# Kernel optimization log

Measured on AMD Instinct MI355X. Metric: run time of the kernel, lower is better.

Reference implementation:

```python
import jax, jax.numpy as jnp
import numpy as np

T, Z, D_DIM = 8, 2048, 1024
N_EXP, P_SLOT, H = 64, 32, 1024
LN_EPS = 1e-5


def setup_inputs() -> dict:
    key = jax.random.key(0)
    k = jax.random.split(key, 5)
    s = 0.02
    return {
        "x": jax.random.normal(k[0], (T, Z, D_DIM), dtype=jnp.float32),
        "phi_w": jax.random.normal(k[1], (N_EXP * P_SLOT, D_DIM), dtype=jnp.float32) * s,
        "phi_b": jax.random.normal(k[2], (N_EXP * P_SLOT,), dtype=jnp.float32) * s,
        "expert_w": jax.random.normal(k[3], (N_EXP, D_DIM, H), dtype=jnp.float32) * s,
        "expert_b": jax.random.normal(k[4], (N_EXP, H), dtype=jnp.float32) * s,
    }


def reference(x, phi_w, phi_b, expert_w, expert_b):
    t, z, d = x.shape
    n = expert_w.shape[0]
    p = phi_w.shape[0] // n
    # routing logits: [t, z, n, p]
    logits = (jnp.einsum('tzd,ed->tze', x, phi_w) + phi_b).reshape(t, z, n, p)
    D = jax.nn.softmax(logits, axis=3)  # dispatch: softmax over slots p
    C = jax.nn.softmax(logits, axis=2)  # combine:  softmax over experts n
    # slot inputs, summed over batch AND tokens (as in the source einsum)
    X_tilde = jnp.einsum('tznp,tzd->npd', D, x)
    X_tilde = jnp.clip(X_tilde, -33000.0, 65000.0)
    # layer norm over last dim, no affine
    mu = jnp.mean(X_tilde, axis=-1, keepdims=True)
    var = jnp.mean(jnp.square(X_tilde - mu), axis=-1, keepdims=True)
    X_tilde = (X_tilde - mu) * jax.lax.rsqrt(var + LN_EPS)
    X_tilde = jnp.tanh(X_tilde)
    # per-expert Linear, batched over experts: [n,p,d] x [n,d,H] -> [n,p,H]
    Y_tilde = jnp.einsum('npd,ndH->npH', X_tilde, expert_w) + expert_b[:, None, :]
    # combine back to tokens: [t,z,H]
    Y = jnp.einsum('tznp,npH->tzH', C, Y_tilde)
    return Y
```

## Files before the change

kernel.cpp:

```cpp
#include <hip/hip_runtime.h>
#include <hip/hip_bf16.h>
#include <math.h>

#define TOKENS   16384
#define DDIM     1024
#define NEXP     64
#define PSLOT    32
#define NSLOTS   2048
#define HDIM     1024
#define LN_EPS   1e-5f
#define KSPLIT   8

typedef __bf16 b16x8 __attribute__((ext_vector_type(8)));
typedef float  f32x4 __attribute__((ext_vector_type(4)));

__device__ __forceinline__ unsigned short f2b(float f) {
    union { float f; unsigned u; } v; v.f = f;
    unsigned r = v.u + 0x7FFF + ((v.u >> 16) & 1);
    return (unsigned short)(r >> 16);
}

__device__ __forceinline__ void load_lds16(const void* g, void* l) {
    __builtin_amdgcn_global_load_lds(
        (const __attribute__((address_space(1))) void*)g,
        (__attribute__((address_space(3))) void*)l, 16, 0, 0);
}

template<bool BIAS>
__global__ __launch_bounds__(512, 2) void gemm_nt_256(
    const unsigned short* __restrict__ A,
    const unsigned short* __restrict__ B,
    const float* __restrict__ bias,
    float* __restrict__ C,
    int M, int N, int K)
{
    __shared__ unsigned short lds[2][2][256 * 64];
    const int tid  = threadIdx.x;
    const int wave = tid >> 6;
    const int lane = tid & 63;
    const int wr = wave >> 2;
    const int wc = wave & 3;
    const int fr = lane & 15;
    const int fs = lane >> 4;
    const int kswz = ((lane & 7) ^ (lane >> 3)) * 8;

    const int gx  = (int)gridDim.x, gy = (int)gridDim.y;
    const int nwg = gx * gy;
    const int wg  = (int)blockIdx.y * gx + (int)blockIdx.x;
    const int swz = (wg & 7) * (nwg >> 3) + (wg >> 3);
    const int m0 = (swz / gx) * 256;
    const int n0 = (swz % gx) * 256;

    const int kc = K / gridDim.z;
    const int kb = blockIdx.z * kc;
    C += (size_t)blockIdx.z * M * N;
    const int NT = kc >> 6;

    f32x4 acc[8][4] = {};
    b16x8 Ag[4][2], Bf[2][2], Bs2[2][2];

#define KOF(T)   (kb + (T) * 64)

#define STAGE_A(BUF, T, R0) { \
    const int k0_ = KOF(T); \
    _Pragma("unroll") for (int hh = 0; hh < 2; ++hh) { \
        const int rp_ = (R0) + hh * 64 + wave * 8 + (lane >> 3); \
        const int L_  = ((rp_ >> 6) & 1) * 128 + ((rp_ >> 7) & 1) * 64 + (rp_ & 63); \
        load_lds16(A + (size_t)(m0 + L_) * K + k0_ + kswz, \
                   &lds[BUF][0][((R0) + hh * 64 + wave * 8) * 64]); } }

#define STAGE_B(BUF, T, R0) { \
    const int k0_ = KOF(T); \
    _Pragma("unroll") for (int hh = 0; hh < 2; ++hh) { \
        const int rp_ = (R0) + hh * 64 + wave * 8 + (lane >> 3); \
        const int L_  = ((rp_ >> 5) & 3) * 64 + ((rp_ >> 7) & 1) * 32 + (rp_ & 31); \
        load_lds16(B + (size_t)(n0 + L_) * K + k0_ + kswz, \
                   &lds[BUF][1][((R0) + hh * 64 + wave * 8) * 64]); } }

#define LDA_G(BUF, IBASE) \
    _Pragma("unroll") for (int ii = 0; ii < 4; ++ii) { \
        const int rp_ = (IBASE) + 64 * wr + ii * 16 + fr; \
        _Pragma("unroll") for (int h = 0; h < 2; ++h) \
            Ag[ii][h] = *(const b16x8*)&lds[BUF][0][rp_ * 64 + (((h * 4 + fs) ^ (rp_ & 7)) * 8)]; }

#define LDB_G(BUF, JBASE, DST) \
    _Pragma("unroll") for (int jj = 0; jj < 2; ++jj) { \
        const int rp_ = (JBASE) + 32 * wc + jj * 16 + fr; \
        _Pragma("unroll") for (int h = 0; h < 2; ++h) \
            DST[jj][h] = *(const b16x8*)&lds[BUF][1][rp_ * 64 + (((h * 4 + fs) ^ (rp_ & 7)) * 8)]; }

#define MFMA_Q(IB, JB, BREG) \
    __builtin_amdgcn_s_setprio(1); \
    _Pragma("unroll") for (int ii = 0; ii < 4; ++ii) \
    _Pragma("unroll") for (int jj = 0; jj < 2; ++jj) \
    _Pragma("unroll") for (int h = 0; h < 2; ++h) \
        acc[(IB) + ii][(JB) + jj] = __builtin_amdgcn_mfma_f32_16x16x32_bf16( \
            Ag[ii][h], BREG[jj][h], acc[(IB) + ii][(JB) + jj], 0, 0, 0); \
    __builtin_amdgcn_s_setprio(0);

#define BAR1  { __builtin_amdgcn_s_barrier(); __builtin_amdgcn_sched_barrier(0); }
#define BAR2  { __builtin_amdgcn_s_barrier(); }
#define VMW6  { asm volatile("s_waitcnt vmcnt(6)" ::: "memory"); \
                __builtin_amdgcn_sched_barrier(0); }
#define VMW0  { asm volatile("s_waitcnt vmcnt(0)" ::: "memory"); \
                __builtin_amdgcn_sched_barrier(0); }

    STAGE_A(0, 0, 0);   STAGE_B(0, 0, 0);   STAGE_B(0, 0, 128);  STAGE_A(0, 0, 128);
    STAGE_A(1, 1, 0);   STAGE_B(1, 1, 0);   STAGE_B(1, 1, 128);
    VMW6; BAR2;

    const int nit = NT >> 1;
    for (int it = 0; it < nit - 1; ++it) {
        const int t1 = 2 * it + 1;
        LDA_G(0, 0); LDB_G(0, 0, Bf);
        STAGE_A(1, t1, 128);
        BAR1; MFMA_Q(0, 0, Bf); BAR2;
        LDB_G(0, 128, Bs2);
        STAGE_A(0, t1 + 1, 0);
        BAR1; MFMA_Q(0, 2, Bs2); BAR2;
        LDA_G(0, 128);
        STAGE_B(0, t1 + 1, 0);
        BAR1; MFMA_Q(4, 2, Bs2); BAR2;
        STAGE_B(0, t1 + 1, 128);
        BAR1; MFMA_Q(4, 0, Bf); VMW6; BAR2;
        LDA_G(1, 0); LDB_G(1, 0, Bf);
        STAGE_A(0, t1 + 1, 128);
        BAR1; MFMA_Q(0, 0, Bf); BAR2;
        LDB_G(1, 128, Bs2);
        STAGE_A(1, t1 + 2, 0);
        BAR1; MFMA_Q(0, 2, Bs2); BAR2;
        LDA_G(1, 128);
        STAGE_B(1, t1 + 2, 0);
        BAR1; MFMA_Q(4, 2, Bs2); BAR2;
        STAGE_B(1, t1 + 2, 128);
        BAR1; MFMA_Q(4, 0, Bf); VMW6; BAR2;
    }

    {
        const int t1 = NT - 1;
        LDA_G(0, 0); LDB_G(0, 0, Bf);
        STAGE_A(1, t1, 128);
        BAR1; MFMA_Q(0, 0, Bf); BAR2;
        LDB_G(0, 128, Bs2);
        BAR1; MFMA_Q(0, 2, Bs2); BAR2;
        LDA_G(0, 128);
        BAR1; MFMA_Q(4, 2, Bs2); BAR2;
        BAR1; MFMA_Q(4, 0, Bf); VMW0; BAR2;
        LDA_G(1, 0); LDB_G(1, 0, Bf);
        BAR1; MFMA_Q(0, 0, Bf); BAR2;
        LDB_G(1, 128, Bs2);
        BAR1; MFMA_Q(0, 2, Bs2); BAR2;
        LDA_G(1, 128);
        BAR1; MFMA_Q(4, 2, Bs2); BAR2;
        BAR1; MFMA_Q(4, 0, Bf); BAR2;
    }

    const int col  = lane & 15;
    const int row4 = (lane >> 4) * 4;
#pragma unroll
    for (int j = 0; j < 4; ++j) {
        const int n = n0 + wc * 64 + j * 16 + col;
        const float bj = BIAS ? bias[n] : 0.f;
#pragma unroll
        for (int i = 0; i < 8; ++i) {
#pragma unroll
            for (int r = 0; r < 4; ++r) {
                const int m = m0 + wr * 128 + i * 16 + row4 + r;
                C[(size_t)m * N + n] = acc[i][j][r] + bj;
            }
        }
    }
#undef KOF
#undef STAGE_A
#undef STAGE_B
#undef LDA_G
#undef LDB_G
#undef MFMA_Q
#undef BAR1
#undef BAR2
#undef VMW6
#undef VMW0
}

__global__ __launch_bounds__(256) void prep_x(
    const float* __restrict__ in, unsigned short* __restrict__ xb,
    unsigned short* __restrict__ xT)
{
    __shared__ unsigned short tile[64][68];
    const int t  = threadIdx.x;
    const int c0 = blockIdx.x * 64;
    const int r0 = blockIdx.y * 64;
    const int tr = t >> 4, tc4 = (t & 15) * 4;
#pragma unroll
    for (int i = 0; i < 4; ++i) {
        const int r = tr + i * 16;
        const float4 v = *(const float4*)&in[(size_t)(r0 + r) * DDIM + c0 + tc4];
        ushort4 o;
        o.x = f2b(v.x); o.y = f2b(v.y); o.z = f2b(v.z); o.w = f2b(v.w);
        *(ushort4*)&xb[(size_t)(r0 + r) * DDIM + c0 + tc4] = o;
        tile[tc4 + 0][r] = o.x; tile[tc4 + 1][r] = o.y;
        tile[tc4 + 2][r] = o.z; tile[tc4 + 3][r] = o.w;
    }
    __syncthreads();
#pragma unroll
    for (int i = 0; i < 4; ++i) {
        const int r = tr + i * 16;
        ushort4 o;
        o.x = tile[r][tc4 + 0]; o.y = tile[r][tc4 + 1];
        o.z = tile[r][tc4 + 2]; o.w = tile[r][tc4 + 3];
        *(ushort4*)&xT[(size_t)(c0 + r) * TOKENS + r0 + tc4] = o;
    }
}

__global__ __launch_bounds__(256) void cast_f32_bf16(
    const float* __restrict__ in, unsigned short* __restrict__ out)
{
    const size_t i = (size_t)(blockIdx.x * 256 + threadIdx.x) * 8;
    const float4 a = *(const float4*)&in[i];
    const float4 b = *(const float4*)&in[i + 4];
    ushort4 o0, o1;
    o0.x = f2b(a.x); o0.y = f2b(a.y); o0.z = f2b(a.z); o0.w = f2b(a.w);
    o1.x = f2b(b.x); o1.y = f2b(b.y); o1.z = f2b(b.z); o1.w = f2b(b.w);
    *(ushort4*)&out[i]     = o0;
    *(ushort4*)&out[i + 4] = o1;
}

__global__ __launch_bounds__(256) void dispatch_T(
    const float* __restrict__ logits, unsigned short* __restrict__ DbT)
{
    __shared__ float ls[8 * 1057];
    const int tid  = threadIdx.x;
    const int tok0 = blockIdx.x * 32;
    const int s0   = blockIdx.y * 256;

#pragma unroll
    for (int i = 0; i < 8; ++i) {
        const int flat = i * 256 + tid;
        const int row  = flat >> 6;
        const int c4   = (flat & 63) * 4;
        const float4 v = *(const float4*)&logits[(size_t)(tok0 + row) * NSLOTS + s0 + c4];
        float* b = &ls[(c4 >> 5) * 1057 + row * 33 + (c4 & 31)];
        b[0] = v.x; b[1] = v.y; b[2] = v.z; b[3] = v.w;
    }
    __syncthreads();

    const int tok = tid & 31, n = tid >> 5;
    const float* r = &ls[n * 1057 + tok * 33];
    float m = r[0];
#pragma unroll
    for (int p = 1; p < PSLOT; ++p) m = fmaxf(m, r[p]);
    float s = 0.f;
#pragma unroll
    for (int p = 0; p < PSLOT; ++p) s += __expf(r[p] - m);
    const float inv = 1.f / s;
    unsigned short* o = &DbT[(size_t)(s0 + n * 32) * TOKENS + tok0 + tok];
#pragma unroll
    for (int p = 0; p < PSLOT; ++p)
        o[(size_t)p * TOKENS] = f2b(__expf(r[p] - m) * inv);
}

__global__ __launch_bounds__(256) void combine_softmax(
    const float* __restrict__ logits, unsigned short* __restrict__ Cb)
{
    __shared__ float ls[NEXP * 33];
    __shared__ float pm[8][32], ps[8][32];
    const int tid = threadIdx.x;
    const size_t base = (size_t)blockIdx.x * NSLOTS;

#pragma unroll
    for (int i = 0; i < 8; ++i) {
        const int e = tid + i * 256;
        ls[e + (e >> 5)] = logits[base + e];
    }
    __syncthreads();

    const int p = tid & 31, sub = tid >> 5;
    float m = ls[(sub * 8) * 33 + p];
#pragma unroll
    for (int k = 1; k < 8; ++k) m = fmaxf(m, ls[(sub * 8 + k) * 33 + p]);
    float s = 0.f;
#pragma unroll
    for (int k = 0; k < 8; ++k) s += __expf(ls[(sub * 8 + k) * 33 + p] - m);
    pm[sub][p] = m; ps[sub][p] = s;
    __syncthreads();

    float M = pm[0][p];
#pragma unroll
    for (int k = 1; k < 8; ++k) M = fmaxf(M, pm[k][p]);
    float S = 0.f;
#pragma unroll
    for (int k = 0; k < 8; ++k) S += ps[k][p] * __expf(pm[k][p] - M);
    const float cinv = 1.f / S;

#pragma unroll
    for (int k = 0; k < 8; ++k) {
        const int n = sub * 8 + k;
        Cb[base + n * 32 + p] = f2b(__expf(ls[n * 33 + p] - M) * cinv);
    }
}

__global__ __launch_bounds__(256) void reduce_ln_tanh(
    const float* __restrict__ parts, float* __restrict__ Xt)
{
    const int tid = threadIdx.x;
    const size_t off = (size_t)blockIdx.x * DDIM + tid * 4;
    __shared__ float red1[4], red2[4];

    float4 v = *(const float4*)&parts[off];
#pragma unroll
    for (int s = 1; s < KSPLIT; ++s) {
        const float4 p = *(const float4*)&parts[(size_t)s * NSLOTS * DDIM + off];
        v.x += p.x; v.y += p.y; v.z += p.z; v.w += p.w;
    }
    v.x = fminf(fmaxf(v.x, -33000.f), 65000.f);
    v.y = fminf(fmaxf(v.y, -33000.f), 65000.f);
    v.z = fminf(fmaxf(v.z, -33000.f), 65000.f);
    v.w = fminf(fmaxf(v.w, -33000.f), 65000.f);

    float s = v.x + v.y + v.z + v.w;
#pragma unroll
    for (int off2 = 32; off2 > 0; off2 >>= 1) s += __shfl_down(s, off2);
    if ((tid & 63) == 0) red1[tid >> 6] = s;
    __syncthreads();
    const float mu = (red1[0] + red1[1] + red1[2] + red1[3]) * (1.f / DDIM);

    const float dx = v.x - mu, dy = v.y - mu, dz = v.z - mu, dw = v.w - mu;
    float q = dx * dx + dy * dy + dz * dz + dw * dw;
#pragma unroll
    for (int off2 = 32; off2 > 0; off2 >>= 1) q += __shfl_down(q, off2);
    if ((tid & 63) == 0) red2[tid >> 6] = q;
    __syncthreads();
    const float var = (red2[0] + red2[1] + red2[2] + red2[3]) * (1.f / DDIM);
    const float sc = rsqrtf(var + LN_EPS);

    float4 o;
    o.x = tanhf(dx * sc); o.y = tanhf(dy * sc);
    o.z = tanhf(dz * sc); o.w = tanhf(dw * sc);
    *(float4*)&Xt[off] = o;
}

__global__ __launch_bounds__(256) void expert_gemm(
    const float* __restrict__ Xt, const float* __restrict__ W,
    const float* __restrict__ bias, unsigned short* __restrict__ YtT)
{
    const int n   = blockIdx.y;
    const int h0  = blockIdx.x * 64;
    const int tid = threadIdx.x;
    __shared__ float As[32][17];
    __shared__ float Bs[16][68];
    __shared__ unsigned short ty[64][36];

    const int r  = tid >> 3;
    const int c8 = (tid & 7) * 8;
    float acc[8];
#pragma unroll
    for (int j = 0; j < 8; ++j) acc[j] = 0.f;

    const float* Wn = W + (size_t)n * DDIM * HDIM;
    for (int k0 = 0; k0 < DDIM; k0 += 16) {
        if (tid < 128) {
            const int row = tid >> 2, c4 = (tid & 3) * 4;
            const float4 v = *(const float4*)&Xt[(size_t)(n * 32 + row) * DDIM + k0 + c4];
            As[row][c4 + 0] = v.x; As[row][c4 + 1] = v.y;
            As[row][c4 + 2] = v.z; As[row][c4 + 3] = v.w;
        }
        {
            const int row = tid >> 4, c4 = (tid & 15) * 4;
            *(float4*)&Bs[row][c4] =
                *(const float4*)&Wn[(size_t)(k0 + row) * HDIM + h0 + c4];
        }
        __syncthreads();
#pragma unroll
        for (int kk = 0; kk < 16; ++kk) {
            const float a = As[r][kk];
            const float4 b0 = *(const float4*)&Bs[kk][c8];
            const float4 b1 = *(const float4*)&Bs[kk][c8 + 4];
            acc[0] = fmaf(a, b0.x, acc[0]); acc[1] = fmaf(a, b0.y, acc[1]);
            acc[2] = fmaf(a, b0.z, acc[2]); acc[3] = fmaf(a, b0.w, acc[3]);
            acc[4] = fmaf(a, b1.x, acc[4]); acc[5] = fmaf(a, b1.y, acc[5]);
            acc[6] = fmaf(a, b1.z, acc[6]); acc[7] = fmaf(a, b1.w, acc[7]);
        }
        __syncthreads();
    }

    const float* bn = bias + (size_t)n * HDIM + h0;
#pragma unroll
    for (int j = 0; j < 8; ++j)
        ty[c8 + j][r] = f2b(acc[j] + bn[c8 + j]);
    __syncthreads();

    const int row = tid >> 2, q = (tid & 3) * 8;
    const ushort4 u0 = *(const ushort4*)&ty[row][q];
    const ushort4 u1 = *(const ushort4*)&ty[row][q + 4];
    unsigned short* dst = &YtT[(size_t)(h0 + row) * NSLOTS + n * 32 + q];
    *(ushort4*)&dst[0] = u0;
    *(ushort4*)&dst[4] = u1;
}

extern "C" void kernel_launch(void* const* d_in, const int* in_sizes, int n_in,
                              void* d_out, int out_size, void* d_ws, size_t ws_size,
                              hipStream_t stream)
{
    const float* x        = (const float*)d_in[0];
    const float* phi_w    = (const float*)d_in[1];
    const float* phi_b    = (const float*)d_in[2];
    const float* expert_w = (const float*)d_in[3];
    const float* expert_b = (const float*)d_in[4];
    float* out = (float*)d_out;

    char* ws = (char*)d_ws;
    const size_t MB = 1u << 20;
    unsigned short* xb     = (unsigned short*)(ws);
    unsigned short* xT     = (unsigned short*)(ws +  32 * MB);
    unsigned short* pwb    = (unsigned short*)(ws +  64 * MB);
    float*          logits = (float*)(ws +  68 * MB);
    unsigned short* DbT    = (unsigned short*)(ws + 196 * MB);
    unsigned short* Cb     = (unsigned short*)(ws + 260 * MB);
    float*          parts  = (float*)(ws + 324 * MB);
    float*          Xt     = (float*)(ws + 388 * MB);
    unsigned short* YtT    = (unsigned short*)(ws + 396 * MB);

    prep_x<<<dim3(DDIM / 64, TOKENS / 64), 256, 0, stream>>>(x, xb, xT);
    cast_f32_bf16<<<NSLOTS * DDIM / (256 * 8), 256, 0, stream>>>(phi_w, pwb);

    gemm_nt_256<true><<<dim3(NSLOTS / 256, TOKENS / 256), 512, 0, stream>>>(
        xb, pwb, phi_b, logits, TOKENS, NSLOTS, DDIM);

    dispatch_T<<<dim3(TOKENS / 32, NSLOTS / 256), 256, 0, stream>>>(logits, DbT);

    combine_softmax<<<TOKENS, 256, 0, stream>>>(logits, Cb);

    gemm_nt_256<false>
        <<<dim3(DDIM / 256, NSLOTS / 256, KSPLIT), 512, 0, stream>>>(
            DbT, xT, nullptr, parts, NSLOTS, DDIM, TOKENS);

    reduce_ln_tanh<<<NSLOTS, 256, 0, stream>>>(parts, Xt);

    expert_gemm<<<dim3(HDIM / 64, NEXP), 256, 0, stream>>>(
        Xt, expert_w, expert_b, YtT);

    gemm_nt_256<false><<<dim3(HDIM / 256, TOKENS / 256), 512, 0, stream>>>(
        Cb, YtT, nullptr, out, TOKENS, HDIM, NSLOTS);
}
```

Baseline: 780.6 us.

## Fuse dispatch and combine softmaxes into one kernel with online expert softmax

```diff
diff --git a/kernel.cpp b/kernel.cpp
--- a/kernel.cpp
+++ b/kernel.cpp
@@ -225,77 +225,93 @@
     *(ushort4*)&out[i + 4] = o1;
 }
 
-__global__ __launch_bounds__(256) void dispatch_T(
-    const float* __restrict__ logits, unsigned short* __restrict__ DbT)
-{
-    __shared__ float ls[8 * 1057];
+__global__ __launch_bounds__(256) void softmax_both(
+    const float* __restrict__ logits,
+    unsigned short* __restrict__ DbT, unsigned short* __restrict__ Cb)
+{
+    __shared__ float ls[8][32][33];
+    __shared__ float Mv[32][33], Sv[32][33];
     const int tid  = threadIdx.x;
     const int tok0 = blockIdx.x * 32;
-    const int s0   = blockIdx.y * 256;
-
-#pragma unroll
-    for (int i = 0; i < 8; ++i) {
-        const int flat = i * 256 + tid;
-        const int row  = flat >> 6;
-        const int c4   = (flat & 63) * 4;
-        const float4 v = *(const float4*)&logits[(size_t)(tok0 + row) * NSLOTS + s0 + c4];
-        float* b = &ls[(c4 >> 5) * 1057 + row * 33 + (c4 & 31)];
-        b[0] = v.x; b[1] = v.y; b[2] = v.z; b[3] = v.w;
-    }
-    __syncthreads();
-
-    const int tok = tid & 31, n = tid >> 5;
-    const float* r = &ls[n * 1057 + tok * 33];
-    float m = r[0];
-#pragma unroll
-    for (int p = 1; p < PSLOT; ++p) m = fmaxf(m, r[p]);
-    float s = 0.f;
-#pragma unroll
-    for (int p = 0; p < PSLOT; ++p) s += __expf(r[p] - m);
-    const float inv = 1.f / s;
-    unsigned short* o = &DbT[(size_t)(s0 + n * 32) * TOKENS + tok0 + tok];
-#pragma unroll
-    for (int p = 0; p < PSLOT; ++p)
-        o[(size_t)p * TOKENS] = f2b(__expf(r[p] - m) * inv);
-}
-
-__global__ __launch_bounds__(256) void combine_softmax(
-    const float* __restrict__ logits, unsigned short* __restrict__ Cb)
-{
-    __shared__ float ls[NEXP * 33];
-    __shared__ float pm[8][32], ps[8][32];
-    const int tid = threadIdx.x;
-    const size_t base = (size_t)blockIdx.x * NSLOTS;
-
-#pragma unroll
-    for (int i = 0; i < 8; ++i) {
-        const int e = tid + i * 256;
-        ls[e + (e >> 5)] = logits[base + e];
-    }
-    __syncthreads();
-
-    const int p = tid & 31, sub = tid >> 5;
-    float m = ls[(sub * 8) * 33 + p];
-#pragma unroll
-    for (int k = 1; k < 8; ++k) m = fmaxf(m, ls[(sub * 8 + k) * 33 + p]);
-    float s = 0.f;
-#pragma unroll
-    for (int k = 0; k < 8; ++k) s += __expf(ls[(sub * 8 + k) * 33 + p] - m);
-    pm[sub][p] = m; ps[sub][p] = s;
-    __syncthreads();
-
-    float M = pm[0][p];
-#pragma unroll
-    for (int k = 1; k < 8; ++k) M = fmaxf(M, pm[k][p]);
-    float S = 0.f;
-#pragma unroll
-    for (int k = 0; k < 8; ++k) S += ps[k][p] * __expf(pm[k][p] - M);
-    const float cinv = 1.f / S;
-
-#pragma unroll
-    for (int k = 0; k < 8; ++k) {
-        const int n = sub * 8 + k;
-        Cb[base + n * 32 + p] = f2b(__expf(ls[n * 33 + p] - M) * cinv);
+    const int tok  = tid & 31;
+
+    {
+        const int tk = tid >> 3, pp = (tid & 7) * 4;
+#pragma unroll
+        for (int q = 0; q < 4; ++q) { Mv[tk][pp + q] = -1e30f; Sv[tk][pp + q] = 0.f; }
+    }
+    __syncthreads();
+
+    for (int c = 0; c < 8; ++c) {
+#pragma unroll
+        for (int i = 0; i < 8; ++i) {
+            const int flat = i * 256 + tid;
+            const int row  = flat >> 6;
+            const int c4   = (flat & 63) * 4;
+            const float4 v = *(const float4*)&logits[(size_t)(tok0 + row) * NSLOTS + c * 256 + c4];
+            float* b = &ls[c4 >> 5][row][c4 & 31];
+            b[0] = v.x; b[1] = v.y; b[2] = v.z; b[3] = v.w;
+        }
+        __syncthreads();
+
+        {
+            const int nl = tid >> 5;
+            const float* r = ls[nl][tok];
+            float m = r[0];
+#pragma unroll
+            for (int p = 1; p < PSLOT; ++p) m = fmaxf(m, r[p]);
+            float s = 0.f;
+#pragma unroll
+            for (int p = 0; p < PSLOT; ++p) s += __expf(r[p] - m);
+            const float inv = 1.f / s;
+            unsigned short* o = &DbT[(size_t)(c * 256 + nl * 32) * TOKENS + tok0 + tok];
+#pragma unroll
+            for (int p = 0; p < PSLOT; ++p)
+                o[(size_t)p * TOKENS] = f2b(__expf(r[p] - m) * inv);
+        }
+
+        {
+            const int pg = tid >> 5;
+#pragma unroll
+            for (int k = 0; k < 4; ++k) {
+                const int p = pg * 4 + k;
+                float m8 = ls[0][tok][p];
+#pragma unroll
+                for (int n = 1; n < 8; ++n) m8 = fmaxf(m8, ls[n][tok][p]);
+                float s8 = 0.f;
+#pragma unroll
+                for (int n = 0; n < 8; ++n) s8 += __expf(ls[n][tok][p] - m8);
+                const float M = Mv[tok][p], S = Sv[tok][p];
+                const float Mn = fmaxf(M, m8);
+                Sv[tok][p] = S * __expf(M - Mn) + s8 * __expf(m8 - Mn);
+                Mv[tok][p] = Mn;
+            }
+        }
+        __syncthreads();
+    }
+
+    {
+        const int tk = tid >> 3, pp = (tid & 7) * 4;
+#pragma unroll
+        for (int q = 0; q < 4; ++q) Sv[tk][pp + q] = 1.f / Sv[tk][pp + q];
+    }
+    __syncthreads();
+
+    for (int c = 0; c < 8; ++c) {
+#pragma unroll
+        for (int i = 0; i < 8; ++i) {
+            const int flat = i * 256 + tid;
+            const int row  = flat >> 6;
+            const int c4   = (flat & 63) * 4;
+            const int p    = c4 & 31;
+            const float4 v = *(const float4*)&logits[(size_t)(tok0 + row) * NSLOTS + c * 256 + c4];
+            ushort4 o;
+            o.x = f2b(__expf(v.x - Mv[row][p + 0]) * Sv[row][p + 0]);
+            o.y = f2b(__expf(v.y - Mv[row][p + 1]) * Sv[row][p + 1]);
+            o.z = f2b(__expf(v.z - Mv[row][p + 2]) * Sv[row][p + 2]);
+            o.w = f2b(__expf(v.w - Mv[row][p + 3]) * Sv[row][p + 3]);
+            *(ushort4*)&Cb[(size_t)(tok0 + row) * NSLOTS + c * 256 + c4] = o;
+        }
     }
 }
 
@@ -426,9 +442,7 @@
     gemm_nt_256<true><<<dim3(NSLOTS / 256, TOKENS / 256), 512, 0, stream>>>(
         xb, pwb, phi_b, logits, TOKENS, NSLOTS, DDIM);
 
-    dispatch_T<<<dim3(TOKENS / 32, NSLOTS / 256), 256, 0, stream>>>(logits, DbT);
-
-    combine_softmax<<<TOKENS, 256, 0, stream>>>(logits, Cb);
+    softmax_both<<<TOKENS / 32, 256, 0, stream>>>(logits, DbT, Cb);
 
     gemm_nt_256<false>
         <<<dim3(DDIM / 256, NSLOTS / 256, KSPLIT), 512, 0, stream>>>(
```

New measurement: 767.4 us. About the same (-1.7%).
